# Kernel tuning notes

Measured on AMD Instinct MI355X. Metric: run time of the kernel, lower is better.

The kernel has to match this reference:

```python
import jax, jax.numpy as jnp
import numpy as np

B, L, E, H = 32, 512, 1024, 1024


def setup_inputs() -> dict:
    key = jax.random.key(0)
    ks = jax.random.split(key, 12)
    s = 0.02
    return {
        "x": jax.random.normal(ks[0], (B, L, E), jnp.float32),
        "h0": jax.random.normal(ks[1], (B, L, H), jnp.float32),
        "c0": jax.random.normal(ks[2], (B, L, H), jnp.float32),
        "W_ioux": jax.random.normal(ks[3], (E, 3 * H), jnp.float32) * s,
        "W_iouh": jax.random.normal(ks[4], (2, H, 3 * H), jnp.float32) * s,
        "b_iouh": jax.random.normal(ks[5], (2, 3 * H), jnp.float32) * s,
        "W_fx": jax.random.normal(ks[6], (E, H), jnp.float32) * s,
        "W_fh": jax.random.normal(ks[7], (4, H, H), jnp.float32) * s,
        "b_fh": jax.random.normal(ks[8], (4, H), jnp.float32) * s,
        "tree_ids_d": jax.random.randint(ks[9], (B, L), 0, L, jnp.int32),
        "tree_ids_dr": jax.random.randint(ks[10], (B, L), 0, L, jnp.int32),
        "tree_ids_dl": jax.random.randint(ks[11], (B, L), 0, L, jnp.int32),
    }


def _scatter_add_rows(src, idx):
    # out[b, idx[b,l], :] += src[b, l, :]   (torch scatter_add_ on dim=1 with row-repeated index)
    b = jnp.arange(src.shape[0])[:, None]
    return jnp.zeros_like(src).at[b, idx].add(src)


def _gather_rows(src, idx):
    # out[b, l, :] = src[b, idx[b,l], :]    (torch gather on dim=1 with row-repeated index)
    return jnp.take_along_axis(src, idx[:, :, None], axis=1)


def _masked_scatter(dest, mask3, src):
    # torch masked_scatter_: True positions (flat order) filled with src elements in flat order
    mflat = mask3.reshape(-1)
    pos = jnp.cumsum(mflat.astype(jnp.int32)) - 1
    filled = jnp.take(src.reshape(-1), jnp.clip(pos, 0, src.size - 1))
    return jnp.where(mflat, filled, dest.reshape(-1)).reshape(dest.shape)


def reference(x, h0, c0, W_ioux, W_iouh, b_iouh, W_fx, W_fh, b_fh,
              tree_ids_d, tree_ids_dr, tree_ids_dl):
    Hh = h0.shape[-1]
    iou_x = x @ W_ioux                               # [B,L,3H]
    iou_hr = h0 @ W_iouh[0] + b_iouh[0]              # [B,L,3H]
    iou_hl = h0 @ W_iouh[1] + b_iouh[1]
    # original repeats index only to hidden_size -> only first H cols (i-gate) get scattered child states
    add = (_scatter_add_rows(iou_hr[..., :Hh], tree_ids_dr)
           + _scatter_add_rows(iou_hl[..., :Hh], tree_ids_dl))
    iou = iou_x.at[..., :Hh].add(add)
    i, o, u = jnp.split(iou, 3, axis=-1)
    i, o, u = jax.nn.sigmoid(i), jax.nn.sigmoid(o), jnp.tanh(u)

    fx = x @ W_fx                                    # [B,L,H]
    # fh[0],fh[1] both gathered at index_r; fh[2],fh[3] both at index_l -> fuse the GEMMs
    fr = h0 @ (W_fh[0] + W_fh[1]) + (b_fh[0] + b_fh[1])
    fl = h0 @ (W_fh[2] + W_fh[3]) + (b_fh[2] + b_fh[3])
    f = jax.nn.sigmoid(_gather_rows(fx, tree_ids_d)
                       + _gather_rows(fr, tree_ids_dr)
                       + _gather_rows(fl, tree_ids_dl))

    fc = f * c0
    c_new = i * u + _scatter_add_rows(fc, tree_ids_d)
    h_new = o * jnp.tanh(c_new)

    mask3 = jnp.broadcast_to((tree_ids_d != 0)[:, :, None], h_new.shape)
    h_out = _masked_scatter(h0, mask3, h_new)
    c_out = _masked_scatter(c0, mask3, c_new)
    return (h_out, c_out)
```

## Files before the change

kernel.cpp:

```cpp
#include <hip/hip_runtime.h>


#define ROWS 16384
#define HID  1024
#define KDIM 1024
#define NCOLS 4096
#define BM 256
#define BN 256

typedef __attribute__((ext_vector_type(4))) int            i32x4;
typedef __attribute__((ext_vector_type(4))) float          f32x4;
typedef __attribute__((ext_vector_type(4))) unsigned short u16x4;
typedef __attribute__((ext_vector_type(8))) unsigned short u16x8;

__device__ __forceinline__ unsigned short f2bf(float f) {
  unsigned u = __float_as_uint(f);
  unsigned r = 0x7FFFu + ((u >> 16) & 1u);
  return (unsigned short)((u + r) >> 16);
}
__device__ __forceinline__ float bf2f(unsigned short v) {
  return __uint_as_float(((unsigned)v) << 16);
}
__device__ __forceinline__ float sigmoidf_(float x) {
  return 1.0f / (1.0f + __expf(-x));
}
__device__ __forceinline__ void gload16(const void* g, void* l) {
  __builtin_amdgcn_global_load_lds(
      (const __attribute__((address_space(1))) void*)g,
      (__attribute__((address_space(3))) void*)l, 16, 0, 0);
}
__device__ __forceinline__ void mfma_bf16(f32x4& acc, i32x4 a, i32x4 b) {
  asm volatile("v_mfma_f32_16x16x32_bf16 %0, %1, %2, %0"
               : "+v"(acc) : "v"(a), "v"(b));
}


__global__ void pack_wx(const float* __restrict__ Wioux, const float* __restrict__ Wfx,
                        unsigned short* __restrict__ Wxt) {
  __shared__ float t[32][33];
  const int n0 = blockIdx.x * 32, k0 = blockIdx.y * 32;
  const int tx = threadIdx.x, ty = threadIdx.y;
  const int n = n0 + tx, k = k0 + ty;
  float v = (n < 3072) ? Wioux[(size_t)k * 3072 + n]
                       : Wfx[(size_t)k * 1024 + (n - 3072)];
  t[ty][tx] = v;
  __syncthreads();
  Wxt[(size_t)(n0 + ty) * KDIM + (k0 + tx)] = f2bf(t[tx][ty]);
}

__global__ void pack_wh(const float* __restrict__ Wiouh, const float* __restrict__ Wfh,
                        unsigned short* __restrict__ Wht) {
  __shared__ float t[32][33];
  const int n0 = blockIdx.x * 32, k0 = blockIdx.y * 32;
  const int tx = threadIdx.x, ty = threadIdx.y;
  const int n = n0 + tx, k = k0 + ty;
  float v;
  if (n < 1024)      v = Wiouh[(size_t)k * 3072 + n];
  else if (n < 2048) v = Wiouh[3145728u + (size_t)k * 3072 + (n - 1024)];
  else if (n < 3072) { const int c = n - 2048;
    v = Wfh[(size_t)k * 1024 + c] + Wfh[1048576u + (size_t)k * 1024 + c]; }
  else { const int c = n - 3072;
    v = Wfh[2097152u + (size_t)k * 1024 + c] + Wfh[3145728u + (size_t)k * 1024 + c]; }
  t[ty][tx] = v;
  __syncthreads();
  Wht[(size_t)(n0 + ty) * KDIM + (k0 + tx)] = f2bf(t[tx][ty]);
}

__global__ void pack_bias(const float* __restrict__ b_iouh, const float* __restrict__ b_fh,
                          float* __restrict__ bh) {
  const int n = blockIdx.x * 1024 + threadIdx.x;
  float v;
  if (n < 1024)      v = b_iouh[n];
  else if (n < 2048) v = b_iouh[3072 + (n - 1024)];
  else if (n < 3072) { const int c = n - 2048; v = b_fh[c] + b_fh[1024 + c]; }
  else { const int c = n - 3072; v = b_fh[2048 + c] + b_fh[3072 + c]; }
  bh[n] = v;
}

__global__ void convert_bf16(const float* __restrict__ x, const float* __restrict__ h0,
                             unsigned short* __restrict__ xb, unsigned short* __restrict__ hb) {
  const size_t i = ((size_t)blockIdx.x * 256 + threadIdx.x) * 4;
  const float4 a = *(const float4*)&x[i];
  const float4 b = *(const float4*)&h0[i];
  u16x4 av = { f2bf(a.x), f2bf(a.y), f2bf(a.z), f2bf(a.w) };
  u16x4 bv = { f2bf(b.x), f2bf(b.y), f2bf(b.z), f2bf(b.w) };
  *(u16x4*)&xb[i] = av;
  *(u16x4*)&hb[i] = bv;
}

__device__ __forceinline__ void stage8(const unsigned short* __restrict__ gp,
                                       unsigned short* __restrict__ lp,
                                       int rowbase, int gbase, int k0, int lane) {
  const int lrow = rowbase + (lane >> 3);
  const int sseg = (lane & 7) ^ ((lane >> 3) & 7);
  gload16(gp + (size_t)(gbase + lrow) * KDIM + k0 + sseg * 8,
          lp + ((size_t)rowbase << 6));
}

#define RD_A(dst, qm)                                                          \
  _Pragma("unroll")                                                            \
  for (int i = 0; i < 4; ++i) {                                                \
    const int row = wr * 128 + (qm) * 64 + i * 16 + m0;                        \
    _Pragma("unroll")                                                          \
    for (int s = 0; s < 2; ++s)                                                \
      dst[i][s] = *(const i32x4*)(Ab + row * 64 + (((kg + s * 4) ^ sw8) << 3)); \
  }

#define RD_B(dst, qn)                                                          \
  _Pragma("unroll")                                                            \
  for (int j = 0; j < 2; ++j) {                                                \
    const int col = wc * 64 + (qn) * 32 + j * 16 + m0;                         \
    _Pragma("unroll")                                                          \
    for (int s = 0; s < 2; ++s)                                                \
      dst[j][s] = *(const i32x4*)(Bb + col * 64 + (((kg + s * 4) ^ sw8) << 3)); \
  }

#define MM(afx, qmb, qnb)                                                      \
  __builtin_amdgcn_s_setprio(1);                                               \
  _Pragma("unroll")                                                            \
  for (int i = 0; i < 4; ++i)                                                  \
    _Pragma("unroll")                                                          \
    for (int j = 0; j < 2; ++j) {                                              \
      mfma_bf16(acc[(qmb) + i][(qnb) + j], afx[i][0], bfr[j][0]);              \
      mfma_bf16(acc[(qmb) + i][(qnb) + j], afx[i][1], bfr[j][1]);              \
    }                                                                          \
  __builtin_amdgcn_s_setprio(0);

__global__ __launch_bounds__(512, 2)
void gemm8(const unsigned short* __restrict__ xb, const unsigned short* __restrict__ hb,
           const unsigned short* __restrict__ Wxt, const unsigned short* __restrict__ Wht,
           unsigned short* __restrict__ gxb, unsigned short* __restrict__ ghb,
           const float* __restrict__ bhv) {
  __shared__ __align__(16) unsigned short S[2][2][256][64];

  const unsigned short* A;
  const unsigned short* Bt;
  unsigned short* Cp;
  const float* bias;
  if (blockIdx.z == 0) { A = xb; Bt = Wxt; Cp = gxb; bias = nullptr; }
  else                 { A = hb; Bt = Wht; Cp = ghb; bias = bhv; }

  int bx = blockIdx.x, by = blockIdx.y;
  const int ny = gridDim.y;
  if ((ny & 7) == 0) {
    const int n = blockIdx.x + 16 * blockIdx.y;
    const int xcd = n & 7, idx = n >> 3;
    const int ych = ny >> 3;
    bx = idx / ych;
    by = xcd * ych + (idx % ych);
  }
  const int bm = by * BM, bn = bx * BN;

  const int tid = threadIdx.x, w = tid >> 6, lane = tid & 63;
  const int wr = w >> 2, wc = w & 3;
  const int m0 = lane & 15, kg = lane >> 4, sw8 = m0 & 7;
  const int bq0 = ((w >> 1) << 6) + ((w & 1) << 4);

  f32x4 acc[8][4] = {};

  stage8(A,  &S[0][0][0][0], w * 8,        bm, 0, lane);
  stage8(A,  &S[0][0][0][0], 128 + w * 8,  bm, 0, lane);
  stage8(A,  &S[0][0][0][0], 64 + w * 8,   bm, 0, lane);
  stage8(A,  &S[0][0][0][0], 192 + w * 8,  bm, 0, lane);
  stage8(Bt, &S[0][1][0][0], bq0,          bn, 0, lane);
  stage8(Bt, &S[0][1][0][0], bq0 + 8,      bn, 0, lane);
  stage8(Bt, &S[0][1][0][0], bq0 + 32,     bn, 0, lane);
  stage8(Bt, &S[0][1][0][0], bq0 + 40,     bn, 0, lane);
  asm volatile("s_waitcnt vmcnt(0)" ::: "memory");
  __builtin_amdgcn_s_barrier();
  __builtin_amdgcn_sched_barrier(0);

  for (int t = 0; t < 16; ++t) {
    const int cur = t & 1, nxt = cur ^ 1;
    const unsigned short* Ab = &S[cur][0][0][0];
    const unsigned short* Bb = &S[cur][1][0][0];
    unsigned short* An = &S[nxt][0][0][0];
    unsigned short* Bn = &S[nxt][1][0][0];
    const int k1 = (t + 1) << 6;
    const bool st = (t < 15);
    i32x4 af0[4][2], af1[4][2], bfr[2][2];

    RD_A(af0, 0)
    RD_B(bfr, 0)
    if (st) { stage8(A, An, w * 8, bm, k1, lane);
              stage8(A, An, 128 + w * 8, bm, k1, lane); }
    MM(af0, 0, 0)

    RD_A(af1, 1)
    if (st) { stage8(Bt, Bn, bq0, bn, k1, lane);
              stage8(Bt, Bn, bq0 + 8, bn, k1, lane); }
    MM(af1, 4, 0)

    RD_B(bfr, 1)
    if (st) { stage8(A, An, 64 + w * 8, bm, k1, lane);
              stage8(A, An, 192 + w * 8, bm, k1, lane); }
    MM(af1, 4, 2)

    if (st) { stage8(Bt, Bn, bq0 + 32, bn, k1, lane);
              stage8(Bt, Bn, bq0 + 40, bn, k1, lane); }
    MM(af0, 0, 2)

    asm volatile("s_waitcnt vmcnt(0) lgkmcnt(0)" ::: "memory");
    __builtin_amdgcn_s_barrier();
    __builtin_amdgcn_sched_barrier(0);
  }

  unsigned short* E = &S[0][0][0][0];
  const int rg = kg * 4;
#pragma unroll
  for (int mi = 0; mi < 8; ++mi) {
#pragma unroll
    for (int nj = 0; nj < 4; ++nj) {
      const int col = wc * 64 + nj * 16 + m0;
      const float bv = bias ? bias[bn + col] : 0.0f;
      const int rowb = wr * 128 + mi * 16 + rg;
#pragma unroll
      for (int r = 0; r < 4; ++r) {
        const int row = rowb + r;
        E[row * 256 + (col ^ (((row >> 2) & 3) << 4))] = f2bf(acc[mi][nj][r] + bv);
      }
    }
  }
  __syncthreads();
#pragma unroll
  for (int jj = 0; jj < 16; ++jj) {
    const int row = jj * 16 + (tid >> 5);
    const int c0 = (tid & 31) * 8;
    const int cs = c0 ^ (((row >> 2) & 3) << 4);
    const u16x8 v = *(const u16x8*)&E[row * 256 + cs];
    *(u16x8*)&Cp[(size_t)(bm + row) * NCOLS + bn + c0] = v;
  }
}

__global__ void scan_mask(const int* __restrict__ idd, int* __restrict__ sel,
                          int* __restrict__ mcount) {
  __shared__ int ps[1024];
  const int t = threadIdx.x;
  int loc[16];
  int cnt = 0;
#pragma unroll
  for (int i = 0; i < 16; ++i) {
    const int v = (idd[t * 16 + i] != 0) ? 1 : 0;
    loc[i] = v; cnt += v;
  }
  ps[t] = cnt;
  __syncthreads();
  for (int off = 1; off < 1024; off <<= 1) {
    const int add = (t >= off) ? ps[t - off] : 0;
    __syncthreads();
    ps[t] += add;
    __syncthreads();
  }
  int rank = (t == 0) ? 0 : ps[t - 1];
#pragma unroll
  for (int i = 0; i < 16; ++i)
    if (loc[i]) sel[rank++] = t * 16 + i;
  if (t == 1023) *mcount = ps[1023];
}

__global__ void build_csr(const int* __restrict__ idd, const int* __restrict__ idr,
                          const int* __restrict__ idl,
                          int* __restrict__ ofsD, int* __restrict__ ofsR, int* __restrict__ ofsL,
                          int* __restrict__ lstD, int* __restrict__ lstR, int* __restrict__ lstL) {
  __shared__ int sidx[512];
  __shared__ int scan[512];
  const int b = blockIdx.x, t = threadIdx.x;
  const int gb = b << 9;
  const int* const srcs[3] = { idd, idr, idl };
  int* const ofss[3] = { ofsD, ofsR, ofsL };
  int* const lsts[3] = { lstD, lstR, lstL };
  for (int a = 0; a < 3; ++a) {
    sidx[t] = srcs[a][gb + t];
    scan[t] = 0;
    __syncthreads();
    atomicAdd(&scan[sidx[t]], 1);
    __syncthreads();
    int v = scan[t];
    for (int off = 1; off < 512; off <<= 1) {
      const int add = (t >= off) ? scan[t - off] : 0;
      __syncthreads();
      scan[t] += add;
      __syncthreads();
    }
    const int start = scan[t] - v;
    ofss[a][b * 513 + t] = start;
    if (t == 511) ofss[a][b * 513 + 512] = scan[511];
    int pos = start;
    for (int l = 0; l < 512; ++l)
      if (sidx[l] == t) lsts[a][gb + (pos++)] = l;
    __syncthreads();
  }
}

__global__ __launch_bounds__(256)
void fused_final(const unsigned short* __restrict__ gxb, const unsigned short* __restrict__ ghb,
                 const float* __restrict__ h0, const float* __restrict__ c0,
                 const int* __restrict__ idd, const int* __restrict__ idr,
                 const int* __restrict__ idl,
                 const int* __restrict__ ofsR, const int* __restrict__ lstR,
                 const int* __restrict__ ofsL, const int* __restrict__ lstL,
                 const int* __restrict__ ofsD, const int* __restrict__ lstD,
                 const int* __restrict__ sel, const int* __restrict__ mcount,
                 float* __restrict__ hout, float* __restrict__ cout, int r0) {
  const int r = blockIdx.x;
  const int g = r0 + r;
  const int j = g & 511;
  const int bb = g >> 9;
  const int lbase = (r >> 9) << 9;
  const int ob = bb * 513;
  const int lb = bb << 9;
  const int c = threadIdx.x << 2;

  float a0 = 0.f, a1 = 0.f, a2 = 0.f, a3 = 0.f;
  for (int q = ofsR[ob + j], e = ofsR[ob + j + 1]; q < e; ++q) {
    const int l = lstR[lb + q];
    const u16x4 v = *(const u16x4*)&ghb[(size_t)(lbase + l) * NCOLS + c];
    a0 += bf2f(v[0]); a1 += bf2f(v[1]); a2 += bf2f(v[2]); a3 += bf2f(v[3]);
  }
  for (int q = ofsL[ob + j], e = ofsL[ob + j + 1]; q < e; ++q) {
    const int l = lstL[lb + q];
    const u16x4 v = *(const u16x4*)&ghb[(size_t)(lbase + l) * NCOLS + 1024 + c];
    a0 += bf2f(v[0]); a1 += bf2f(v[1]); a2 += bf2f(v[2]); a3 += bf2f(v[3]);
  }

  const u16x4 fx4 = *(const u16x4*)&gxb[(size_t)r * NCOLS + 3072 + c];
  const float fx0 = bf2f(fx4[0]), fx1 = bf2f(fx4[1]), fx2 = bf2f(fx4[2]), fx3 = bf2f(fx4[3]);
  float fc0 = 0.f, fc1 = 0.f, fc2 = 0.f, fc3 = 0.f;
  for (int q = ofsD[ob + j], e = ofsD[ob + j + 1]; q < e; ++q) {
    const int l = lstD[lb + q];
    const int jr = idr[lb + l], jl = idl[lb + l];
    const u16x4 rv = *(const u16x4*)&ghb[(size_t)(lbase + jr) * NCOLS + 2048 + c];
    const u16x4 lv = *(const u16x4*)&ghb[(size_t)(lbase + jl) * NCOLS + 3072 + c];
    const float4 cc = *(const float4*)&c0[(size_t)(lb + l) * HID + c];
    fc0 += sigmoidf_(fx0 + bf2f(rv[0]) + bf2f(lv[0])) * cc.x;
    fc1 += sigmoidf_(fx1 + bf2f(rv[1]) + bf2f(lv[1])) * cc.y;
    fc2 += sigmoidf_(fx2 + bf2f(rv[2]) + bf2f(lv[2])) * cc.z;
    fc3 += sigmoidf_(fx3 + bf2f(rv[3]) + bf2f(lv[3])) * cc.w;
  }

  const u16x4 vi = *(const u16x4*)&gxb[(size_t)r * NCOLS + c];
  const u16x4 vo = *(const u16x4*)&gxb[(size_t)r * NCOLS + 1024 + c];
  const u16x4 vu = *(const u16x4*)&gxb[(size_t)r * NCOLS + 2048 + c];
  float4 hn, cn;
  {
    const float ig = sigmoidf_(bf2f(vi[0]) + a0), og = sigmoidf_(bf2f(vo[0]));
    cn.x = ig * tanhf(bf2f(vu[0])) + fc0; hn.x = og * tanhf(cn.x);
  }
  {
    const float ig = sigmoidf_(bf2f(vi[1]) + a1), og = sigmoidf_(bf2f(vo[1]));
    cn.y = ig * tanhf(bf2f(vu[1])) + fc1; hn.y = og * tanhf(cn.y);
  }
  {
    const float ig = sigmoidf_(bf2f(vi[2]) + a2), og = sigmoidf_(bf2f(vo[2]));
    cn.z = ig * tanhf(bf2f(vu[2])) + fc2; hn.z = og * tanhf(cn.z);
  }
  {
    const float ig = sigmoidf_(bf2f(vi[3]) + a3), og = sigmoidf_(bf2f(vo[3]));
    cn.w = ig * tanhf(bf2f(vu[3])) + fc3; hn.w = og * tanhf(cn.w);
  }

  if (idd[g] == 0) {
    *(float4*)&hout[(size_t)g * HID + c] = *(const float4*)&h0[(size_t)g * HID + c];
    *(float4*)&cout[(size_t)g * HID + c] = *(const float4*)&c0[(size_t)g * HID + c];
  }
  const int m = *mcount;
  if (g < m) {
    const int o = sel[g];
    *(float4*)&hout[(size_t)o * HID + c] = hn;
    *(float4*)&cout[(size_t)o * HID + c] = cn;
  }
}

extern "C" void kernel_launch(void* const* d_in, const int* in_sizes, int n_in,
                              void* d_out, int out_size, void* d_ws, size_t ws_size,
                              hipStream_t stream) {
  const float* x      = (const float*)d_in[0];
  const float* h0     = (const float*)d_in[1];
  const float* c0     = (const float*)d_in[2];
  const float* W_ioux = (const float*)d_in[3];
  const float* W_iouh = (const float*)d_in[4];
  const float* b_iouh = (const float*)d_in[5];
  const float* W_fx   = (const float*)d_in[6];
  const float* W_fh   = (const float*)d_in[7];
  const float* b_fh   = (const float*)d_in[8];
  const int* idd      = (const int*)d_in[9];
  const int* idr      = (const int*)d_in[10];
  const int* idl      = (const int*)d_in[11];
  float* hout = (float*)d_out;
  float* cout = hout + (size_t)ROWS * HID;

  char* ws = (char*)d_ws;
  unsigned short* Wxt  = (unsigned short*)(ws);
  unsigned short* Wht  = (unsigned short*)(ws + 8388608u);
  float*          bh   = (float*)(ws + 16777216u);
  int*            sel  = (int*)(ws + 16793600u);
  int*            mcnt = (int*)(ws + 16859136u);
  int*            ofsD = (int*)(ws + 16859392u);
  int*            ofsR = (int*)(ws + 16925184u);
  int*            ofsL = (int*)(ws + 16990976u);
  int*            lstD = (int*)(ws + 17056768u);
  int*            lstR = (int*)(ws + 17122304u);
  int*            lstL = (int*)(ws + 17187840u);
  const size_t    base = 17253376u;

  int C = 32;
  while (C > 1 && base + 10485760ull * (size_t)C > ws_size) C >>= 1;
  const int R = 512 * C;

  char* p = ws + base;
  unsigned short* xb  = (unsigned short*)p;  p += 1048576ull * C;
  unsigned short* hb  = (unsigned short*)p;  p += 1048576ull * C;
  unsigned short* gxb = (unsigned short*)p;  p += 4194304ull * C;
  unsigned short* ghb = (unsigned short*)p;

  pack_wx<<<dim3(128, 32), dim3(32, 32), 0, stream>>>(W_ioux, W_fx, Wxt);
  pack_wh<<<dim3(128, 32), dim3(32, 32), 0, stream>>>(W_iouh, W_fh, Wht);
  pack_bias<<<4, 1024, 0, stream>>>(b_iouh, b_fh, bh);
  scan_mask<<<1, 1024, 0, stream>>>(idd, sel, mcnt);
  build_csr<<<32, 512, 0, stream>>>(idd, idr, idl, ofsD, ofsR, ofsL, lstD, lstR, lstL);

  for (int b0 = 0; b0 < 32; b0 += C) {
    const size_t r0 = (size_t)b0 * 512;
    convert_bf16<<<R, 256, 0, stream>>>(x + r0 * HID, h0 + r0 * HID, xb, hb);
    gemm8<<<dim3(NCOLS / BN, R / BM, 2), 512, 0, stream>>>(xb, hb, Wxt, Wht, gxb, ghb, bh);
    fused_final<<<R, 256, 0, stream>>>(gxb, ghb, h0, c0, idd, idr, idl,
                                       ofsR, lstR, ofsL, lstL, ofsD, lstD,
                                       sel, mcnt, hout, cout, (int)r0);
  }
}
```

Baseline: 548.7 us.

## Switch GEMM to 4-slot BK=32 LDS ring with 3-stage prefetch

Replaces the double-buffered BK=64 main loop with a four-slot ring of BK=32 tiles. Loads run three stages ahead and partial vmcnt waits replace the full drain each iteration. The goal is to hide global-load latency better and avoid stalling on vmcnt(0) every step. In exchange there are twice as many K iterations and barriers, and a new staging and swizzle layout that has to match the reads exactly.

Measured after the change: 547.0 us. No clear change (-0.3%).

```diff
diff --git a/kernel.cpp b/kernel.cpp
--- a/kernel.cpp
+++ b/kernel.cpp
@@ -88,42 +88,36 @@
   *(u16x4*)&hb[i] = bv;
 }
 
-__device__ __forceinline__ void stage8(const unsigned short* __restrict__ gp,
-                                       unsigned short* __restrict__ lp,
-                                       int rowbase, int gbase, int k0, int lane) {
-  const int lrow = rowbase + (lane >> 3);
-  const int sseg = (lane & 7) ^ ((lane >> 3) & 7);
-  gload16(gp + (size_t)(gbase + lrow) * KDIM + k0 + sseg * 8,
-          lp + ((size_t)rowbase << 6));
-}
-
-#define RD_A(dst, qm)                                                          \
+__device__ __forceinline__ void stageR(const unsigned short* __restrict__ gp,
+                                       unsigned short* __restrict__ slot,
+                                       int rb, int gbase, int k0, int tid) {
+  const int r = rb + (tid >> 2);
+  const int sseg = (tid & 3) ^ (r & 3);
+  unsigned short* lp = slot + (size_t)(rb + ((tid >> 6) << 4)) * 32;
+  gload16(gp + (size_t)(gbase + r) * KDIM + k0 + sseg * 8, lp);
+}
+
+#define RD_A(qm)                                                               \
   _Pragma("unroll")                                                            \
   for (int i = 0; i < 4; ++i) {                                                \
-    const int row = wr * 128 + (qm) * 64 + i * 16 + m0;                        \
-    _Pragma("unroll")                                                          \
-    for (int s = 0; s < 2; ++s)                                                \
-      dst[i][s] = *(const i32x4*)(Ab + row * 64 + (((kg + s * 4) ^ sw8) << 3)); \
-  }
-
-#define RD_B(dst, qn)                                                          \
+    const int R = wr * 128 + (qm) * 64 + i * 16 + m0;                          \
+    af[i] = *(const i32x4*)(Ab + R * 32 + ((kg ^ sw) << 3));                   \
+  }
+
+#define RD_B                                                                   \
   _Pragma("unroll")                                                            \
-  for (int j = 0; j < 2; ++j) {                                                \
-    const int col = wc * 64 + (qn) * 32 + j * 16 + m0;                         \
-    _Pragma("unroll")                                                          \
-    for (int s = 0; s < 2; ++s)                                                \
-      dst[j][s] = *(const i32x4*)(Bb + col * 64 + (((kg + s * 4) ^ sw8) << 3)); \
-  }
-
-#define MM(afx, qmb, qnb)                                                      \
+  for (int j = 0; j < 4; ++j) {                                                \
+    const int Cc = wc * 64 + j * 16 + m0;                                      \
+    bfr[j] = *(const i32x4*)(Bb + Cc * 32 + ((kg ^ sw) << 3));                 \
+  }
+
+#define MM(qmb)                                                                \
   __builtin_amdgcn_s_setprio(1);                                               \
   _Pragma("unroll")                                                            \
   for (int i = 0; i < 4; ++i)                                                  \
     _Pragma("unroll")                                                          \
-    for (int j = 0; j < 2; ++j) {                                              \
-      mfma_bf16(acc[(qmb) + i][(qnb) + j], afx[i][0], bfr[j][0]);              \
-      mfma_bf16(acc[(qmb) + i][(qnb) + j], afx[i][1], bfr[j][1]);              \
-    }                                                                          \
+    for (int j = 0; j < 4; ++j)                                                \
+      mfma_bf16(acc[(qmb) + i][j], af[i], bfr[j]);                             \
   __builtin_amdgcn_s_setprio(0);
 
 __global__ __launch_bounds__(512, 2)
@@ -131,7 +125,7 @@
            const unsigned short* __restrict__ Wxt, const unsigned short* __restrict__ Wht,
            unsigned short* __restrict__ gxb, unsigned short* __restrict__ ghb,
            const float* __restrict__ bhv) {
-  __shared__ __align__(16) unsigned short S[2][2][256][64];
+  __shared__ __align__(16) unsigned short S[4][2][256][32];
 
   const unsigned short* A;
   const unsigned short* Bt;
@@ -153,58 +147,51 @@
 
   const int tid = threadIdx.x, w = tid >> 6, lane = tid & 63;
   const int wr = w >> 2, wc = w & 3;
-  const int m0 = lane & 15, kg = lane >> 4, sw8 = m0 & 7;
-  const int bq0 = ((w >> 1) << 6) + ((w & 1) << 4);
+  const int m0 = lane & 15, kg = lane >> 4, sw = m0 & 3;
 
   f32x4 acc[8][4] = {};
 
-  stage8(A,  &S[0][0][0][0], w * 8,        bm, 0, lane);
-  stage8(A,  &S[0][0][0][0], 128 + w * 8,  bm, 0, lane);
-  stage8(A,  &S[0][0][0][0], 64 + w * 8,   bm, 0, lane);
-  stage8(A,  &S[0][0][0][0], 192 + w * 8,  bm, 0, lane);
-  stage8(Bt, &S[0][1][0][0], bq0,          bn, 0, lane);
-  stage8(Bt, &S[0][1][0][0], bq0 + 8,      bn, 0, lane);
-  stage8(Bt, &S[0][1][0][0], bq0 + 32,     bn, 0, lane);
-  stage8(Bt, &S[0][1][0][0], bq0 + 40,     bn, 0, lane);
-  asm volatile("s_waitcnt vmcnt(0)" ::: "memory");
+  for (int tt = 0; tt < 3; ++tt) {
+    stageR(A,  &S[tt][0][0][0], 0,   bm, tt * 32, tid);
+    stageR(A,  &S[tt][0][0][0], 128, bm, tt * 32, tid);
+    stageR(Bt, &S[tt][1][0][0], 0,   bn, tt * 32, tid);
+    stageR(Bt, &S[tt][1][0][0], 128, bn, tt * 32, tid);
+  }
+  asm volatile("s_waitcnt vmcnt(8)" ::: "memory");
   __builtin_amdgcn_s_barrier();
   __builtin_amdgcn_sched_barrier(0);
 
-  for (int t = 0; t < 16; ++t) {
-    const int cur = t & 1, nxt = cur ^ 1;
-    const unsigned short* Ab = &S[cur][0][0][0];
-    const unsigned short* Bb = &S[cur][1][0][0];
-    unsigned short* An = &S[nxt][0][0][0];
-    unsigned short* Bn = &S[nxt][1][0][0];
-    const int k1 = (t + 1) << 6;
-    const bool st = (t < 15);
-    i32x4 af0[4][2], af1[4][2], bfr[2][2];
-
-    RD_A(af0, 0)
-    RD_B(bfr, 0)
-    if (st) { stage8(A, An, w * 8, bm, k1, lane);
-              stage8(A, An, 128 + w * 8, bm, k1, lane); }
-    MM(af0, 0, 0)
-
-    RD_A(af1, 1)
-    if (st) { stage8(Bt, Bn, bq0, bn, k1, lane);
-              stage8(Bt, Bn, bq0 + 8, bn, k1, lane); }
-    MM(af1, 4, 0)
-
-    RD_B(bfr, 1)
-    if (st) { stage8(A, An, 64 + w * 8, bm, k1, lane);
-              stage8(A, An, 192 + w * 8, bm, k1, lane); }
-    MM(af1, 4, 2)
-
-    if (st) { stage8(Bt, Bn, bq0 + 32, bn, k1, lane);
-              stage8(Bt, Bn, bq0 + 40, bn, k1, lane); }
-    MM(af0, 0, 2)
-
-    asm volatile("s_waitcnt vmcnt(0) lgkmcnt(0)" ::: "memory");
-    __builtin_amdgcn_s_barrier();
-    __builtin_amdgcn_sched_barrier(0);
-  }
-
+  for (int t = 0; t < 32; ++t) {
+    const int sl = t & 3;
+    const unsigned short* Ab = &S[sl][0][0][0];
+    const unsigned short* Bb = &S[sl][1][0][0];
+    const bool st = (t < 29);
+    const int sl3 = (t + 3) & 3;
+    const int k3 = (t + 3) << 5;
+    i32x4 af[4], bfr[4];
+
+    RD_A(0)
+    RD_B
+    if (st) { stageR(A,  &S[sl3][0][0][0], 0, bm, k3, tid);
+              stageR(Bt, &S[sl3][1][0][0], 0, bn, k3, tid); }
+    MM(0)
+
+    RD_A(1)
+    if (st) { stageR(A,  &S[sl3][0][0][0], 128, bm, k3, tid);
+              stageR(Bt, &S[sl3][1][0][0], 128, bn, k3, tid); }
+    MM(4)
+
+    if (t <= 28)      asm volatile("s_waitcnt vmcnt(8)" ::: "memory");
+    else if (t == 29) asm volatile("s_waitcnt vmcnt(4)" ::: "memory");
+    else if (t == 30) asm volatile("s_waitcnt vmcnt(0)" ::: "memory");
+    if (t < 31) {
+      __builtin_amdgcn_s_barrier();
+      __builtin_amdgcn_sched_barrier(0);
+    }
+  }
+
+  __builtin_amdgcn_s_barrier();
+  __builtin_amdgcn_sched_barrier(0);
   unsigned short* E = &S[0][0][0][0];
   const int rg = kg * 4;
 #pragma unroll
```
